# Kernel optimization log

Hardware: AMD Instinct MI355X
Metric: run time of the kernel (lower is better)

## Reference

```python
import jax, jax.numpy as jnp
import numpy as np

N = 4096
INP_DIM = 256
EMB_DIM = 256
ALPHA = 0.01  # LeakyReLU negative slope
NEG_INF = -9.0e15


def _xavier(key, shape, gain=1.414):
    fan_in, fan_out = shape[0], shape[1]
    limit = gain * np.sqrt(6.0 / (fan_in + fan_out))
    return jax.random.uniform(key, shape, jnp.float32, -limit, limit)


def setup_inputs() -> dict:
    key = jax.random.key(0)
    ks = jax.random.split(key, 9)
    inp = {
        "input": jax.random.normal(ks[0], (N, INP_DIM), jnp.float32),
        "adj": jax.random.randint(ks[1], (N, N), 0, 2, jnp.int32),
        "W0": _xavier(ks[2], (INP_DIM, EMB_DIM)),
        "W1": _xavier(ks[3], (EMB_DIM, EMB_DIM)),
        "a1": _xavier(ks[4], (2 * EMB_DIM, 1)),
        "W2": _xavier(ks[5], (EMB_DIM, EMB_DIM)),
        "a2": _xavier(ks[6], (2 * EMB_DIM, 1)),
        "W3": _xavier(ks[7], (EMB_DIM, EMB_DIM)),
        "a3": _xavier(ks[8], (2 * EMB_DIM, 1)),
    }
    return inp


def _gat_layer(h, adj, W, a):
    # h: [N, F_in], W: [F_in, F], a: [2F, 1]
    Wh = h @ W                       # [N, F]
    F_out = Wh.shape[1]
    # e_ij = leakyrelu([Wh_i || Wh_j] @ a) = leakyrelu(Wh_i@a1 + Wh_j@a2)
    f1 = Wh @ a[:F_out]              # [N, 1]
    f2 = Wh @ a[F_out:]              # [N, 1]
    e = jax.nn.leaky_relu(f1 + f2.T, ALPHA)            # [N, N]
    att = jnp.where(adj > 0, e, NEG_INF)
    att = jax.nn.softmax(att, axis=1)                    # masked softmax over neighbors
    h_prime = att @ Wh                                   # [N, F]
    return jax.nn.elu(h_prime)                           # concat=True -> ELU


def reference(input, adj, W0, W1, a1, W2, a2, W3, a3):
    h = input @ W0                   # GAT-level projection
    h = _gat_layer(h, adj, W1, a1)
    h = _gat_layer(h, adj, W2, a2)
    h = _gat_layer(h, adj, W3, a3)
    return h
```

## Files before the change

kernel.cpp:

```cpp
#include <hip/hip_runtime.h>
#include <hip/hip_bf16.h>
#include <cstdint>
#include <cstddef>

#define NN 4096
#define FD 256
#define WPR 64

typedef __attribute__((ext_vector_type(8))) unsigned short ushort8v;
typedef __attribute__((ext_vector_type(4))) unsigned short ushort4v;
typedef __attribute__((ext_vector_type(8))) short short8;
typedef __attribute__((ext_vector_type(4))) float float4v;

static __device__ __forceinline__ unsigned short f2bf(float x) {
    union { float f; unsigned int u; } v; v.f = x;
    unsigned int r = v.u + 0x7FFFu + ((v.u >> 16) & 1u);
    return (unsigned short)(r >> 16);
}

static __device__ __forceinline__ short8 as_s8(ushort8v v) {
    union { ushort8v u; short8 s; } x; x.u = v; return x.s;
}

__global__ __launch_bounds__(256) void pack_adj(const int* __restrict__ adj,
                                                unsigned long long* __restrict__ bits) {
    const int row = blockIdx.x;
    const int t = threadIdx.x;
    const int wave = t >> 6, lane = t & 63;
    const int* arow = adj + (size_t)row * NN;
    #pragma unroll
    for (int it = 0; it < NN / 256; ++it) {
        int j = it * 256 + wave * 64 + lane;
        unsigned long long m = __ballot(arow[j] > 0);
        if (lane == 0) bits[(size_t)row * WPR + (it * 4 + wave)] = m;
    }
}

__global__ __launch_bounds__(256) void cvt_w(const float* __restrict__ W0, const float* __restrict__ W1,
                                             const float* __restrict__ W2, const float* __restrict__ W3,
                                             unsigned short* __restrict__ Wbt) {
    int idx = blockIdx.x * 256 + threadIdx.x;
    int mat = idx >> 16;
    int within = idx & 65535;
    int n = within >> 8, k = within & 255;
    const float* W = (mat == 0) ? W0 : (mat == 1) ? W1 : (mat == 2) ? W2 : W3;
    Wbt[idx] = f2bf(W[k * 256 + n]);
}

__global__ __launch_bounds__(256) void cvt_h(const float* __restrict__ x, unsigned short* __restrict__ hb) {
    int idx = blockIdx.x * 256 + threadIdx.x;
    hb[idx] = f2bf(x[idx]);
}

__global__ __launch_bounds__(256) void proj_gemm(const unsigned short* __restrict__ A,
                                                 const unsigned short* __restrict__ Bt,
                                                 float* __restrict__ Cf,
                                                 unsigned short* __restrict__ Cbt,
                                                 unsigned short* __restrict__ Crow) {
    const int t = threadIdx.x;
    const int bm = blockIdx.x >> 2, bn = blockIdx.x & 3;
    const int m0 = bm * 64, n0 = bn * 64;
    __shared__ unsigned short smem[64 * 40 * 2];
    unsigned short* As = smem;
    unsigned short* Bs = smem + 64 * 40;
    const int lane = t & 63, wave = t >> 6;
    const int wm = (wave >> 1) * 32, wn = (wave & 1) * 32;
    const int sr = t >> 2, sc = (t & 3) * 8;
    float4v acc[2][2] = {{{0.f,0.f,0.f,0.f},{0.f,0.f,0.f,0.f}},{{0.f,0.f,0.f,0.f},{0.f,0.f,0.f,0.f}}};

    for (int kk = 0; kk < 256; kk += 32) {
        *(ushort8v*)&As[sr * 40 + sc] = *(const ushort8v*)&A[(size_t)(m0 + sr) * 256 + kk + sc];
        *(ushort8v*)&Bs[sr * 40 + sc] = *(const ushort8v*)&Bt[(size_t)(n0 + sr) * 256 + kk + sc];
        __syncthreads();
        const int kc = (lane >> 4) * 8;
        #pragma unroll
        for (int fm = 0; fm < 2; ++fm) {
            short8 a = as_s8(*(const ushort8v*)&As[(wm + fm * 16 + (lane & 15)) * 40 + kc]);
            #pragma unroll
            for (int fn = 0; fn < 2; ++fn) {
                short8 b = as_s8(*(const ushort8v*)&Bs[(wn + fn * 16 + (lane & 15)) * 40 + kc]);
                acc[fm][fn] = __builtin_amdgcn_mfma_f32_16x16x32_bf16(a, b, acc[fm][fn], 0, 0, 0);
            }
        }
        __syncthreads();
    }

    const int rb = wm + (lane >> 4) * 4;
    const int cb = wn + (lane & 15);
    #pragma unroll
    for (int fm = 0; fm < 2; ++fm)
        #pragma unroll
        for (int fn = 0; fn < 2; ++fn)
            #pragma unroll
            for (int r = 0; r < 4; ++r) {
                int lr = rb + fm * 16 + r;
                int lc = cb + fn * 16;
                float v = acc[fm][fn][r];
                if (Cf)   Cf[(size_t)(m0 + lr) * 256 + n0 + lc] = v;
                if (Crow) Crow[(size_t)(m0 + lr) * 256 + n0 + lc] = f2bf(v);
            }

    if (Cbt) {
        unsigned short* T = smem;
        #pragma unroll
        for (int fm = 0; fm < 2; ++fm)
            #pragma unroll
            for (int fn = 0; fn < 2; ++fn)
                #pragma unroll
                for (int r = 0; r < 4; ++r)
                    T[(cb + fn * 16) * 72 + rb + fm * 16 + r] = f2bf(acc[fm][fn][r]);
        __syncthreads();
        const int tr = t >> 2;
        #pragma unroll
        for (int i = 0; i < 2; ++i) {
            int tc = (t & 3) * 8 + i * 32;
            *(ushort8v*)&Cbt[(size_t)(n0 + tr) * 4096 + m0 + tc] = *(const ushort8v*)&T[tr * 72 + tc];
        }
    }
}

__global__ __launch_bounds__(256) void fvec(const float* __restrict__ Wh, const float* __restrict__ a,
                                            float* __restrict__ f1, float* __restrict__ f2) {
    const int wave = threadIdx.x >> 6, lane = threadIdx.x & 63;
    const int i = blockIdx.x * 4 + wave;
    const float* row = Wh + (size_t)i * 256;
    float s1 = 0.f, s2 = 0.f;
    #pragma unroll
    for (int c0 = 0; c0 < 256; c0 += 64) {
        int c = c0 + lane;
        float w = row[c];
        s1 += w * a[c];
        s2 += w * a[256 + c];
    }
    #pragma unroll
    for (int off = 32; off > 0; off >>= 1) {
        s1 += __shfl_down(s1, off, 64);
        s2 += __shfl_down(s2, off, 64);
    }
    if (lane == 0) { f1[i] = s1; f2[i] = s2; }
}

__global__ __launch_bounds__(256) void stats(const unsigned long long* __restrict__ bits,
                                             const float* __restrict__ f1, const float* __restrict__ f2,
                                             float* __restrict__ rowmax, float* __restrict__ invsum) {
    const int i = blockIdx.x;
    const int t = threadIdx.x;
    __shared__ unsigned long long wbits[WPR];
    __shared__ float red_m[256], red_s[256];
    if (t < WPR) wbits[t] = bits[(size_t)i * WPR + t];
    __syncthreads();
    const float f1i = f1[i];
    float m = -3.0e38f, s = 0.f;
    #pragma unroll
    for (int it = 0; it < 16; ++it) {
        int j = it * 256 + t;
        if ((wbits[j >> 6] >> (j & 63)) & 1ULL) {
            float e = f1i + f2[j];
            e = e > 0.f ? e : 0.01f * e;
            if (e > m) { s = s * __expf(m - e) + 1.f; m = e; }
            else       { s += __expf(e - m); }
        }
    }
    red_m[t] = m; red_s[t] = s;
    __syncthreads();
    for (int off = 128; off > 0; off >>= 1) {
        if (t < off) {
            float m2 = red_m[t + off], s2 = red_s[t + off];
            float mo = red_m[t], so = red_s[t];
            float mn = fmaxf(mo, m2);
            red_s[t] = so * __expf(mo - mn) + s2 * __expf(m2 - mn);
            red_m[t] = mn;
        }
        __syncthreads();
    }
    if (t == 0) { rowmax[i] = red_m[0]; invsum[i] = 1.0f / red_s[0]; }
}

__global__ __launch_bounds__(256, 2) void att_split(const unsigned long long* __restrict__ bits,
                                                    const float* __restrict__ f1, const float* __restrict__ f2,
                                                    const float* __restrict__ rowmax,
                                                    const unsigned short* __restrict__ Bt,
                                                    float* __restrict__ part, int kchunk) {
    const int t = threadIdx.x;
    const int bm = blockIdx.x & 63;
    const int ks = blockIdx.x >> 6;
    const int m0 = bm * 64;
    const int k0 = ks * kchunk;
    __shared__ unsigned short As[64 * 40];
    __shared__ unsigned short Bs[256 * 40];
    const int lane = t & 63, wave = t >> 6;
    const int wn = wave * 64;
    const int sr = t >> 2, sc = (t & 3) * 8;
    const float f1r = f1[m0 + sr];
    const float mr = rowmax[m0 + sr];
    const unsigned long long* brow = bits + (size_t)(m0 + sr) * WPR;
    float4v acc[4][4];
    #pragma unroll
    for (int i = 0; i < 4; ++i)
        #pragma unroll
        for (int j = 0; j < 4; ++j) acc[i][j] = (float4v){0.f, 0.f, 0.f, 0.f};

    for (int kk = k0; kk < k0 + kchunk; kk += 32) {
        unsigned long long w = brow[kk >> 6];
        const int sb = (kk & 63) + sc;
        float4v fa = *(const float4v*)&f2[kk + sc];
        float4v fb = *(const float4v*)&f2[kk + sc + 4];
        ushort8v pa;
        #pragma unroll
        for (int jj = 0; jj < 8; ++jj) {
            float e = f1r + ((jj < 4) ? fa[jj] : fb[jj - 4]);
            e = e > 0.f ? e : 0.01f * e;
            float p = ((w >> (sb + jj)) & 1ULL) ? __expf(e - mr) : 0.f;
            pa[jj] = f2bf(p);
        }
        *(ushort8v*)&As[sr * 40 + sc] = pa;
        #pragma unroll
        for (int i = 0; i < 4; ++i) {
            int r = i * 64 + sr;
            *(ushort8v*)&Bs[r * 40 + sc] = *(const ushort8v*)&Bt[(size_t)r * 4096 + kk + sc];
        }
        __syncthreads();
        const int kc = (lane >> 4) * 8;
        short8 a[4], b[4];
        #pragma unroll
        for (int fm = 0; fm < 4; ++fm)
            a[fm] = as_s8(*(const ushort8v*)&As[(fm * 16 + (lane & 15)) * 40 + kc]);
        #pragma unroll
        for (int fn = 0; fn < 4; ++fn)
            b[fn] = as_s8(*(const ushort8v*)&Bs[(wn + fn * 16 + (lane & 15)) * 40 + kc]);
        #pragma unroll
        for (int fm = 0; fm < 4; ++fm)
            #pragma unroll
            for (int fn = 0; fn < 4; ++fn)
                acc[fm][fn] = __builtin_amdgcn_mfma_f32_16x16x32_bf16(a[fm], b[fn], acc[fm][fn], 0, 0, 0);
        __syncthreads();
    }

    const int rb = (lane >> 4) * 4;
    const int cb = wn + (lane & 15);
    float* pbase = part + ((size_t)ks << 20);
    #pragma unroll
    for (int fm = 0; fm < 4; ++fm)
        #pragma unroll
        for (int fn = 0; fn < 4; ++fn)
            #pragma unroll
            for (int r = 0; r < 4; ++r)
                pbase[(size_t)(m0 + rb + fm * 16 + r) * 256 + cb + fn * 16] = acc[fm][fn][r];
}

__global__ __launch_bounds__(256) void att_reduce(const float* __restrict__ part,
                                                  const float* __restrict__ invsum,
                                                  float* __restrict__ outf,
                                                  unsigned short* __restrict__ hrow, int nsplit) {
    const int idx = (blockIdx.x * 256 + threadIdx.x) * 4;
    const int m = idx >> 8;
    float4v s = *(const float4v*)&part[idx];
    for (int sp = 1; sp < nsplit; ++sp)
        s += *(const float4v*)&part[((size_t)sp << 20) + idx];
    const float inv = invsum[m];
    float4v v;
    ushort4v hb;
    #pragma unroll
    for (int j = 0; j < 4; ++j) {
        float x = s[j] * inv;
        x = x > 0.f ? x : (__expf(x) - 1.f);
        v[j] = x;
        hb[j] = f2bf(x);
    }
    if (outf) *(float4v*)&outf[idx] = v;
    *(ushort4v*)&hrow[idx] = hb;
}

extern "C" void kernel_launch(void* const* d_in, const int* in_sizes, int n_in,
                              void* d_out, int out_size, void* d_ws, size_t ws_size,
                              hipStream_t stream) {
    const float* input = (const float*)d_in[0];
    const int*   adj   = (const int*)d_in[1];
    const float* W0    = (const float*)d_in[2];
    const float* W1    = (const float*)d_in[3];
    const float* a1    = (const float*)d_in[4];
    const float* W2    = (const float*)d_in[5];
    const float* a2    = (const float*)d_in[6];
    const float* W3    = (const float*)d_in[7];
    const float* a3    = (const float*)d_in[8];
    float* out = (float*)d_out;
    char* ws = (char*)d_ws;

    unsigned long long* bits = (unsigned long long*)(ws);
    unsigned short* h0   = (unsigned short*)(ws + (2u << 20));
    unsigned short* h1   = (unsigned short*)(ws + (4u << 20));
    unsigned short* Whbt = (unsigned short*)(ws + (6u << 20));
    float*          Whf  = (float*)(ws + (8u << 20));
    unsigned short* Wbt  = (unsigned short*)(ws + (12u << 20));
    float* f1v   = (float*)(ws + (12u << 20) + (512u << 10));
    float* f2v   = f1v + 4096;
    float* rmax  = f2v + 4096;
    float* isum  = rmax + 4096;
    float* part  = (float*)(ws + (13u << 20));

    const size_t base = 13u << 20;
    int SPLIT = 8;
    while (SPLIT > 1 && base + (size_t)SPLIT * (4u << 20) > ws_size) SPLIT >>= 1;
    const int kchunk = NN / SPLIT;

    pack_adj<<<4096, 256, 0, stream>>>(adj, bits);
    cvt_w<<<1024, 256, 0, stream>>>(W0, W1, W2, W3, Wbt);
    cvt_h<<<4096, 256, 0, stream>>>(input, h0);

    proj_gemm<<<256, 256, 0, stream>>>(h0, Wbt + 0 * 65536, nullptr, nullptr, h1);

    proj_gemm<<<256, 256, 0, stream>>>(h1, Wbt + 1 * 65536, Whf, Whbt, nullptr);
    fvec<<<1024, 256, 0, stream>>>(Whf, a1, f1v, f2v);
    stats<<<4096, 256, 0, stream>>>(bits, f1v, f2v, rmax, isum);
    att_split<<<64 * SPLIT, 256, 0, stream>>>(bits, f1v, f2v, rmax, Whbt, part, kchunk);
    att_reduce<<<1024, 256, 0, stream>>>(part, isum, nullptr, h0, SPLIT);

    proj_gemm<<<256, 256, 0, stream>>>(h0, Wbt + 2 * 65536, Whf, Whbt, nullptr);
    fvec<<<1024, 256, 0, stream>>>(Whf, a2, f1v, f2v);
    stats<<<4096, 256, 0, stream>>>(bits, f1v, f2v, rmax, isum);
    att_split<<<64 * SPLIT, 256, 0, stream>>>(bits, f1v, f2v, rmax, Whbt, part, kchunk);
    att_reduce<<<1024, 256, 0, stream>>>(part, isum, nullptr, h1, SPLIT);

    proj_gemm<<<256, 256, 0, stream>>>(h1, Wbt + 3 * 65536, Whf, Whbt, nullptr);
    fvec<<<1024, 256, 0, stream>>>(Whf, a3, f1v, f2v);
    stats<<<4096, 256, 0, stream>>>(bits, f1v, f2v, rmax, isum);
    att_split<<<64 * SPLIT, 256, 0, stream>>>(bits, f1v, f2v, rmax, Whbt, part, kchunk);
    att_reduce<<<1024, 256, 0, stream>>>(part, isum, out, h0, SPLIT);
}
```

Baseline: 296.0 us.

## Factor exp(leakyrelu(f1+f2)) into per-column tables and per-row coefficients

```diff
diff --git a/kernel.cpp b/kernel.cpp
--- a/kernel.cpp
+++ b/kernel.cpp
@@ -11,6 +11,9 @@
 typedef __attribute__((ext_vector_type(4))) unsigned short ushort4v;
 typedef __attribute__((ext_vector_type(8))) short short8;
 typedef __attribute__((ext_vector_type(4))) float float4v;
+
+#define C1 30.0f
+#define C2 0.3f
 
 static __device__ __forceinline__ unsigned short f2bf(float x) {
     union { float f; unsigned int u; } v; v.f = x;
@@ -60,29 +63,31 @@
     const int t = threadIdx.x;
     const int bm = blockIdx.x >> 2, bn = blockIdx.x & 3;
     const int m0 = bm * 64, n0 = bn * 64;
-    __shared__ unsigned short smem[64 * 40 * 2];
-    unsigned short* As = smem;
-    unsigned short* Bs = smem + 64 * 40;
+    __shared__ unsigned short As[64 * 264];
+    __shared__ unsigned short Bs[64 * 264];
     const int lane = t & 63, wave = t >> 6;
     const int wm = (wave >> 1) * 32, wn = (wave & 1) * 32;
-    const int sr = t >> 2, sc = (t & 3) * 8;
+    const int lr = t >> 2, lc0 = (t & 3) * 8;
+    #pragma unroll
+    for (int i = 0; i < 8; ++i) {
+        int col = lc0 + i * 32;
+        *(ushort8v*)&As[lr * 264 + col] = *(const ushort8v*)&A[(size_t)(m0 + lr) * 256 + col];
+        *(ushort8v*)&Bs[lr * 264 + col] = *(const ushort8v*)&Bt[(size_t)(n0 + lr) * 256 + col];
+    }
+    __syncthreads();
     float4v acc[2][2] = {{{0.f,0.f,0.f,0.f},{0.f,0.f,0.f,0.f}},{{0.f,0.f,0.f,0.f},{0.f,0.f,0.f,0.f}}};
-
+    #pragma unroll
     for (int kk = 0; kk < 256; kk += 32) {
-        *(ushort8v*)&As[sr * 40 + sc] = *(const ushort8v*)&A[(size_t)(m0 + sr) * 256 + kk + sc];
-        *(ushort8v*)&Bs[sr * 40 + sc] = *(const ushort8v*)&Bt[(size_t)(n0 + sr) * 256 + kk + sc];
-        __syncthreads();
-        const int kc = (lane >> 4) * 8;
+        const int kc = kk + (lane >> 4) * 8;
         #pragma unroll
         for (int fm = 0; fm < 2; ++fm) {
-            short8 a = as_s8(*(const ushort8v*)&As[(wm + fm * 16 + (lane & 15)) * 40 + kc]);
+            short8 a = as_s8(*(const ushort8v*)&As[(wm + fm * 16 + (lane & 15)) * 264 + kc]);
             #pragma unroll
             for (int fn = 0; fn < 2; ++fn) {
-                short8 b = as_s8(*(const ushort8v*)&Bs[(wn + fn * 16 + (lane & 15)) * 40 + kc]);
+                short8 b = as_s8(*(const ushort8v*)&Bs[(wn + fn * 16 + (lane & 15)) * 264 + kc]);
                 acc[fm][fn] = __builtin_amdgcn_mfma_f32_16x16x32_bf16(a, b, acc[fm][fn], 0, 0, 0);
             }
         }
-        __syncthreads();
     }
 
     const int rb = wm + (lane >> 4) * 4;
@@ -93,15 +98,16 @@
         for (int fn = 0; fn < 2; ++fn)
             #pragma unroll
             for (int r = 0; r < 4; ++r) {
-                int lr = rb + fm * 16 + r;
-                int lc = cb + fn * 16;
+                int lr2 = rb + fm * 16 + r;
+                int lc2 = cb + fn * 16;
                 float v = acc[fm][fn][r];
-                if (Cf)   Cf[(size_t)(m0 + lr) * 256 + n0 + lc] = v;
-                if (Crow) Crow[(size_t)(m0 + lr) * 256 + n0 + lc] = f2bf(v);
+                if (Cf)   Cf[(size_t)(m0 + lr2) * 256 + n0 + lc2] = v;
+                if (Crow) Crow[(size_t)(m0 + lr2) * 256 + n0 + lc2] = f2bf(v);
             }
 
     if (Cbt) {
-        unsigned short* T = smem;
+        unsigned short* T = As;
+        __syncthreads();
         #pragma unroll
         for (int fm = 0; fm < 2; ++fm)
             #pragma unroll
@@ -120,7 +126,7 @@
 }
 
 __global__ __launch_bounds__(256) void fvec(const float* __restrict__ Wh, const float* __restrict__ a,
-                                            float* __restrict__ f1, float* __restrict__ f2) {
+                                            float* __restrict__ f1, float* __restrict__ tabf) {
     const int wave = threadIdx.x >> 6, lane = threadIdx.x & 63;
     const int i = blockIdx.x * 4 + wave;
     const float* row = Wh + (size_t)i * 256;
@@ -137,48 +143,61 @@
         s1 += __shfl_down(s1, off, 64);
         s2 += __shfl_down(s2, off, 64);
     }
-    if (lane == 0) { f1[i] = s1; f2[i] = s2; }
-}
-
-__global__ __launch_bounds__(256) void stats(const unsigned long long* __restrict__ bits,
-                                             const float* __restrict__ f1, const float* __restrict__ f2,
-                                             float* __restrict__ rowmax, float* __restrict__ invsum) {
-    const int i = blockIdx.x;
+    if (lane == 0) {
+        f1[i] = s1;
+        tabf[2 * i]     = __expf(s2 - C1);
+        tabf[2 * i + 1] = __expf(0.01f * s2 - C2);
+    }
+}
+
+__global__ __launch_bounds__(256) void rowcoef(const unsigned long long* __restrict__ bits,
+                                               const float* __restrict__ f1,
+                                               const float2* __restrict__ tab,
+                                               float4* __restrict__ rowco) {
+    __shared__ float2 tl[4096];
     const int t = threadIdx.x;
-    __shared__ unsigned long long wbits[WPR];
-    __shared__ float red_m[256], red_s[256];
-    if (t < WPR) wbits[t] = bits[(size_t)i * WPR + t];
+    #pragma unroll
+    for (int i = 0; i < 16; ++i) tl[i * 256 + t] = tab[i * 256 + t];
     __syncthreads();
-    const float f1i = f1[i];
-    float m = -3.0e38f, s = 0.f;
-    #pragma unroll
-    for (int it = 0; it < 16; ++it) {
-        int j = it * 256 + t;
-        if ((wbits[j >> 6] >> (j & 63)) & 1ULL) {
-            float e = f1i + f2[j];
-            e = e > 0.f ? e : 0.01f * e;
-            if (e > m) { s = s * __expf(m - e) + 1.f; m = e; }
-            else       { s += __expf(e - m); }
-        }
-    }
-    red_m[t] = m; red_s[t] = s;
-    __syncthreads();
-    for (int off = 128; off > 0; off >>= 1) {
-        if (t < off) {
-            float m2 = red_m[t + off], s2 = red_s[t + off];
-            float mo = red_m[t], so = red_s[t];
-            float mn = fmaxf(mo, m2);
-            red_s[t] = so * __expf(mo - mn) + s2 * __expf(m2 - mn);
-            red_m[t] = mn;
-        }
-        __syncthreads();
-    }
-    if (t == 0) { rowmax[i] = red_m[0]; invsum[i] = 1.0f / red_s[0]; }
+    const int lane = t & 63, wave = t >> 6;
+    for (int rr = 0; rr < 2; ++rr) {
+        const int row = blockIdx.x * 8 + wave * 2 + rr;
+        const unsigned long long wl = bits[(size_t)row * WPR + lane];
+        const float f1r = f1[row];
+        const float th = __expf(-f1r - C1);
+        float mx = 0.f, S1 = 0.f, S2 = 0.f;
+        #pragma unroll 16
+        for (int b = 0; b < 64; ++b) {
+            unsigned long long w = __shfl(wl, b, 64);
+            bool bit = (w >> lane) & 1ULL;
+            float2 v = tl[b * 64 + lane];
+            float ebm = bit ? v.x : 0.f;
+            mx = fmaxf(mx, ebm);
+            bool cond = v.x > th;
+            S1 += (bit && cond)  ? v.x : 0.f;
+            S2 += (bit && !cond) ? v.y : 0.f;
+        }
+        #pragma unroll
+        for (int off = 1; off < 64; off <<= 1) {
+            mx = fmaxf(mx, __shfl_xor(mx, off, 64));
+            S1 += __shfl_xor(S1, off, 64);
+            S2 += __shfl_xor(S2, off, 64);
+        }
+        if (lane == 0) {
+            float M  = C1 + __logf(mx);
+            float fm_ = f1r + M;
+            float m  = fm_ > 0.f ? fm_ : 0.01f * fm_;
+            float alpha = __expf(fminf(f1r + C1 - m, 60.f));
+            float gamma = __expf(fminf(0.01f * (f1r + C1) - m, 60.f));
+            float inv = 1.0f / (alpha * S1 + gamma * S2);
+            rowco[row] = make_float4(alpha * inv, gamma * inv, th, 0.f);
+        }
+    }
 }
 
 __global__ __launch_bounds__(256, 2) void att_split(const unsigned long long* __restrict__ bits,
-                                                    const float* __restrict__ f1, const float* __restrict__ f2,
-                                                    const float* __restrict__ rowmax,
+                                                    const float4* __restrict__ rowco,
+                                                    const float* __restrict__ tabf,
                                                     const unsigned short* __restrict__ Bt,
                                                     float* __restrict__ part, int kchunk) {
     const int t = threadIdx.x;
@@ -186,13 +205,13 @@
     const int ks = blockIdx.x >> 6;
     const int m0 = bm * 64;
     const int k0 = ks * kchunk;
-    __shared__ unsigned short As[64 * 40];
-    __shared__ unsigned short Bs[256 * 40];
+    __shared__ unsigned short As[64 * 72];
+    __shared__ unsigned short Bs[256 * 72];
     const int lane = t & 63, wave = t >> 6;
     const int wn = wave * 64;
-    const int sr = t >> 2, sc = (t & 3) * 8;
-    const float f1r = f1[m0 + sr];
-    const float mr = rowmax[m0 + sr];
+    const int sr = t >> 2, q = t & 3, sc = q * 16;
+    const float4 rc = rowco[m0 + sr];
+    const float pA = rc.x, pG = rc.y, th = rc.z;
     const unsigned long long* brow = bits + (size_t)(m0 + sr) * WPR;
     float4v acc[4][4];
     #pragma unroll
@@ -200,39 +219,53 @@
         #pragma unroll
         for (int j = 0; j < 4; ++j) acc[i][j] = (float4v){0.f, 0.f, 0.f, 0.f};
 
-    for (int kk = k0; kk < k0 + kchunk; kk += 32) {
-        unsigned long long w = brow[kk >> 6];
-        const int sb = (kk & 63) + sc;
-        float4v fa = *(const float4v*)&f2[kk + sc];
-        float4v fb = *(const float4v*)&f2[kk + sc + 4];
-        ushort8v pa;
-        #pragma unroll
-        for (int jj = 0; jj < 8; ++jj) {
-            float e = f1r + ((jj < 4) ? fa[jj] : fb[jj - 4]);
-            e = e > 0.f ? e : 0.01f * e;
-            float p = ((w >> (sb + jj)) & 1ULL) ? __expf(e - mr) : 0.f;
-            pa[jj] = f2bf(p);
-        }
-        *(ushort8v*)&As[sr * 40 + sc] = pa;
+    for (int kk = k0; kk < k0 + kchunk; kk += 64) {
+        const unsigned int wb = (unsigned int)(brow[kk >> 6] >> sc) & 0xFFFFu;
+        float tv[32];
+        {
+            const float4v* tp = (const float4v*)&tabf[2 * (kk + sc)];
+            #pragma unroll
+            for (int i = 0; i < 8; ++i) {
+                float4v x = tp[i];
+                tv[4 * i] = x[0]; tv[4 * i + 1] = x[1]; tv[4 * i + 2] = x[2]; tv[4 * i + 3] = x[3];
+            }
+        }
+        ushort8v pa0, pa1;
+        #pragma unroll
+        for (int jj = 0; jj < 16; ++jj) {
+            float eb = tv[2 * jj], ed = tv[2 * jj + 1];
+            bool cond = eb > th;
+            float val  = cond ? eb : ed;
+            float coef = cond ? pA : pG;
+            float p = ((wb >> jj) & 1u) ? coef * val : 0.f;
+            unsigned short pb = f2bf(p);
+            if (jj < 8) pa0[jj] = pb; else pa1[jj - 8] = pb;
+        }
+        *(ushort8v*)&As[sr * 72 + sc]     = pa0;
+        *(ushort8v*)&As[sr * 72 + sc + 8] = pa1;
         #pragma unroll
         for (int i = 0; i < 4; ++i) {
             int r = i * 64 + sr;
-            *(ushort8v*)&Bs[r * 40 + sc] = *(const ushort8v*)&Bt[(size_t)r * 4096 + kk + sc];
+            *(ushort8v*)&Bs[r * 72 + sc]     = *(const ushort8v*)&Bt[(size_t)r * 4096 + kk + sc];
+            *(ushort8v*)&Bs[r * 72 + sc + 8] = *(const ushort8v*)&Bt[(size_t)r * 4096 + kk + sc + 8];
         }
         __syncthreads();
-        const int kc = (lane >> 4) * 8;
-        short8 a[4], b[4];
-        #pragma unroll
-        for (int fm = 0; fm < 4; ++fm)
-            a[fm] = as_s8(*(const ushort8v*)&As[(fm * 16 + (lane & 15)) * 40 + kc]);
-        #pragma unroll
-        for (int fn = 0; fn < 4; ++fn)
-            b[fn] = as_s8(*(const ushort8v*)&Bs[(wn + fn * 16 + (lane & 15)) * 40 + kc]);
-        #pragma unroll
-        for (int fm = 0; fm < 4; ++fm)
+        #pragma unroll
+        for (int half = 0; half < 2; ++half) {
+            const int kc = half * 32 + (lane >> 4) * 8;
+            short8 a[4], b[4];
+            #pragma unroll
+            for (int fm = 0; fm < 4; ++fm)
+                a[fm] = as_s8(*(const ushort8v*)&As[(fm * 16 + (lane & 15)) * 72 + kc]);
             #pragma unroll
             for (int fn = 0; fn < 4; ++fn)
-                acc[fm][fn] = __builtin_amdgcn_mfma_f32_16x16x32_bf16(a[fm], b[fn], acc[fm][fn], 0, 0, 0);
+                b[fn] = as_s8(*(const ushort8v*)&Bs[(wn + fn * 16 + (lane & 15)) * 72 + kc]);
+            #pragma unroll
+            for (int fm = 0; fm < 4; ++fm)
+                #pragma unroll
+                for (int fn = 0; fn < 4; ++fn)
+                    acc[fm][fn] = __builtin_amdgcn_mfma_f32_16x16x32_bf16(a[fm], b[fn], acc[fm][fn], 0, 0, 0);
+        }
         __syncthreads();
     }
 
@@ -249,20 +282,17 @@
 }
 
 __global__ __launch_bounds__(256) void att_reduce(const float* __restrict__ part,
-                                                  const float* __restrict__ invsum,
                                                   float* __restrict__ outf,
                                                   unsigned short* __restrict__ hrow, int nsplit) {
     const int idx = (blockIdx.x * 256 + threadIdx.x) * 4;
-    const int m = idx >> 8;
     float4v s = *(const float4v*)&part[idx];
     for (int sp = 1; sp < nsplit; ++sp)
         s += *(const float4v*)&part[((size_t)sp << 20) + idx];
-    const float inv = invsum[m];
     float4v v;
     ushort4v hb;
     #pragma unroll
     for (int j = 0; j < 4; ++j) {
-        float x = s[j] * inv;
+        float x = s[j];
         x = x > 0.f ? x : (__expf(x) - 1.f);
         v[j] = x;
         hb[j] = f2bf(x);
@@ -292,11 +322,10 @@
     unsigned short* Whbt = (unsigned short*)(ws + (6u << 20));
     float*          Whf  = (float*)(ws + (8u << 20));
     unsigned short* Wbt  = (unsigned short*)(ws + (12u << 20));
-    float* f1v   = (float*)(ws + (12u << 20) + (512u << 10));
-    float* f2v   = f1v + 4096;
-    float* rmax  = f2v + 4096;
-    float* isum  = rmax + 4096;
-    float* part  = (float*)(ws + (13u << 20));
+    float*  f1v   = (float*)(ws + (12u << 20) + (512u << 10));
+    float*  tabf  = f1v + 4096;
+    float4* rowco = (float4*)(tabf + 8192);
+    float*  part  = (float*)(ws + (13u << 20));
 
     const size_t base = 13u << 20;
     int SPLIT = 8;
@@ -310,20 +339,20 @@
     proj_gemm<<<256, 256, 0, stream>>>(h0, Wbt + 0 * 65536, nullptr, nullptr, h1);
 
     proj_gemm<<<256, 256, 0, stream>>>(h1, Wbt + 1 * 65536, Whf, Whbt, nullptr);
-    fvec<<<1024, 256, 0, stream>>>(Whf, a1, f1v, f2v);
-    stats<<<4096, 256, 0, stream>>>(bits, f1v, f2v, rmax, isum);
-    att_split<<<64 * SPLIT, 256, 0, stream>>>(bits, f1v, f2v, rmax, Whbt, part, kchunk);
-    att_reduce<<<1024, 256, 0, stream>>>(part, isum, nullptr, h0, SPLIT);
+    fvec<<<1024, 256, 0, stream>>>(Whf, a1, f1v, tabf);
+    rowcoef<<<512, 256, 0, stream>>>(bits, f1v, (const float2*)tabf, rowco);
+    att_split<<<64 * SPLIT, 256, 0, stream>>>(bits, rowco, tabf, Whbt, part, kchunk);
+    att_reduce<<<1024, 256, 0, stream>>>(part, nullptr, h0, SPLIT);
 
     proj_gemm<<<256, 256, 0, stream>>>(h0, Wbt + 2 * 65536, Whf, Whbt, nullptr);
-    fvec<<<1024, 256, 0, stream>>>(Whf, a2, f1v, f2v);
-    stats<<<4096, 256, 0, stream>>>(bits, f1v, f2v, rmax, isum);
-    att_split<<<64 * SPLIT, 256, 0, stream>>>(bits, f1v, f2v, rmax, Whbt, part, kchunk);
-    att_reduce<<<1024, 256, 0, stream>>>(part, isum, nullptr, h1, SPLIT);
+    fvec<<<1024, 256, 0, stream>>>(Whf, a2, f1v, tabf);
+    rowcoef<<<512, 256, 0, stream>>>(bits, f1v, (const float2*)tabf, rowco);
+    att_split<<<64 * SPLIT, 256, 0, stream>>>(bits, rowco, tabf, Whbt, part, kchunk);
+    att_reduce<<<1024, 256, 0, stream>>>(part, nullptr, h1, SPLIT);
 
     proj_gemm<<<256, 256, 0, stream>>>(h1, Wbt + 3 * 65536, Whf, Whbt, nullptr);
-    fvec<<<1024, 256, 0, stream>>>(Whf, a3, f1v, f2v);
-    stats<<<4096, 256, 0, stream>>>(bits, f1v, f2v, rmax, isum);
-    att_split<<<64 * SPLIT, 256, 0, stream>>>(bits, f1v, f2v, rmax, Whbt, part, kchunk);
-    att_reduce<<<1024, 256, 0, stream>>>(part, isum, out, h0, SPLIT);
-}
+    fvec<<<1024, 256, 0, stream>>>(Whf, a3, f1v, tabf);
+    rowcoef<<<512, 256, 0, stream>>>(bits, f1v, (const float2*)tabf, rowco);
+    att_split<<<64 * SPLIT, 256, 0, stream>>>(bits, rowco, tabf, Whbt, part, kchunk);
+    att_reduce<<<1024, 256, 0, stream>>>(part, out, h0, SPLIT);
+}
```

Result: faster. 289.9 us (-2.1%).
